# Kernel optimization log

Measured on AMD Instinct MI355X. Metric: run time of the kernel, lower is better.

## Reference

```python
import jax, jax.numpy as jnp
import numpy as np

A = 128      # attention_dim
E = 512      # embedding_dim
NF = 32      # attention_location_n_filters
K = 31       # attention_location_kernel_size
B, T = 64, 1024


def setup_inputs() -> dict:
    key = jax.random.key(0)
    ks = jax.random.split(key, 10)
    inp = {
        "attention_hidden_state": jax.random.normal(ks[0], (B, A), jnp.float32),
        "memory": jax.random.normal(ks[1], (B, T, E), jnp.float32),
        "processed_memory": jax.random.normal(ks[2], (B, T, E), jnp.float32),
        "attention_weights_cat": jax.random.uniform(ks[3], (B, 2, T), jnp.float32),
        "mask": jax.random.randint(ks[4], (B, T), 0, 2).astype(bool),
        # parameters (torch Linear weight layout [out, in], Conv1d [out, in, k])
        "Wq": jax.random.normal(ks[5], (A, A), jnp.float32) / np.sqrt(A),
        "Wm": jax.random.normal(ks[6], (A, E), jnp.float32) / np.sqrt(E),
        "v": jax.random.normal(ks[7], (1, A), jnp.float32) / np.sqrt(A),
        "conv_w": jax.random.normal(ks[8], (NF, 2, K), jnp.float32) / np.sqrt(2 * K),
        "Wl": jax.random.normal(ks[9], (A, NF), jnp.float32) / np.sqrt(NF),
    }
    return inp


def reference(attention_hidden_state, memory, processed_memory,
              attention_weights_cat, mask, Wq, Wm, v, conv_w, Wl):
    # processed_query: [B, 1, A]
    pq = (attention_hidden_state @ Wq.T)[:, None, :]
    # processed_memory through memory_layer: [B, T, A]
    pm = jnp.einsum('bte,ae->bta', processed_memory, Wm)
    # location conv: [B, 2, T] -> [B, NF, T], SAME padding ((K-1)//2)
    pad = (K - 1) // 2
    loc = jax.lax.conv_general_dilated(
        attention_weights_cat, conv_w,
        window_strides=(1,), padding=[(pad, pad)],
        dimension_numbers=('NCH', 'OIH', 'NCH'))
    # [B, T, NF] -> location_layer -> [B, T, A]
    pa = jnp.einsum('bft,af->bta', loc, Wl)
    # energies: [B, T]
    energies = jnp.einsum('bta,a->bt', jnp.tanh(pq + pm + pa), v[0])
    energies = jnp.where(mask, -jnp.inf, energies)
    attention_weights = jax.nn.softmax(energies, axis=1)
    # context: [B, E]
    attention_context = jnp.einsum('bt,bte->be', attention_weights, memory)
    return attention_context, attention_weights
```

## Files before the change

kernel.cpp:

```cpp
#include <hip/hip_runtime.h>
#include <stdint.h>

#define A_DIM 128
#define E_DIM 512
#define NFLT  32
#define KW    31
#define BATCH 64
#define T_DIM 1024

typedef short short8 __attribute__((ext_vector_type(8)));
typedef float float4v __attribute__((ext_vector_type(4)));

__device__ __forceinline__ unsigned short f2bf(float f) {
    union { float f; unsigned int u; } x; x.f = f;
    unsigned int u = x.u;
    return (unsigned short)((u + 0x7fffu + ((u >> 16) & 1u)) >> 16);
}

__global__ __launch_bounds__(256) void prep_kernel(
    const float* __restrict__ hidden, const float* __restrict__ Wq,
    const float* __restrict__ Wm, const float* __restrict__ Wl,
    unsigned short* __restrict__ Wm_bf, unsigned short* __restrict__ Wl_bf,
    float* __restrict__ pq)
{
    int idx = blockIdx.x * 256 + threadIdx.x;
    if (idx < A_DIM * E_DIM) {
        Wm_bf[idx] = f2bf(Wm[idx]);
    } else if (idx < A_DIM * E_DIM + A_DIM * NFLT) {
        int i = idx - A_DIM * E_DIM;
        Wl_bf[i] = f2bf(Wl[i]);
    } else if (idx < A_DIM * E_DIM + A_DIM * NFLT + BATCH * A_DIM) {
        int i = idx - (A_DIM * E_DIM + A_DIM * NFLT);
        int b = i >> 7, a = i & 127;
        const float* h = hidden + b * A_DIM;
        const float* wq = Wq + a * A_DIM;
        float s = 0.f;
        for (int j = 0; j < A_DIM; ++j) s += h[j] * wq[j];
        pq[i] = s;
    }
}

__global__ __launch_bounds__(256) void detect_mask_kernel(
    const unsigned int* __restrict__ mw, int* __restrict__ flag)
{
    __shared__ unsigned int red[256];
    unsigned int f = 0;
    for (int i = threadIdx.x; i < 16384; i += 256) {
        unsigned int v = mw[i];
        if (v == 0x3F800000u) f |= 1u;
        else if (v > 1u) f |= 2u;
    }
    red[threadIdx.x] = f;
    __syncthreads();
    for (int s = 128; s > 0; s >>= 1) {
        if (threadIdx.x < (unsigned)s) red[threadIdx.x] |= red[threadIdx.x + s];
        __syncthreads();
    }
    if (threadIdx.x == 0) {
        unsigned int r = red[0];
        flag[0] = (r & 1u) ? 2 : ((r & 2u) ? 1 : 0);
    }
}

__global__ __launch_bounds__(256) void energies_kernel(
    const float* __restrict__ P,
    const float* __restrict__ awcat,
    const float* __restrict__ convw,
    const unsigned short* __restrict__ Wm_bf,
    const unsigned short* __restrict__ Wl_bf,
    const float* __restrict__ pq,
    const float* __restrict__ vvec,
    float* __restrict__ energies)
{
    const int tid = threadIdx.x;
    const int b  = blockIdx.x >> 3;
    const int t0 = (blockIdx.x & 7) << 7;

    __shared__ float aw_lds[2][160];
    __shared__ unsigned short loc_lds[128][NFLT];

    for (int i = tid; i < 320; i += 256) {
        int c = i / 160, j = i % 160;
        int tg = t0 - 15 + j;
        float vl = 0.f;
        if (j < 158 && tg >= 0 && tg < T_DIM) vl = awcat[(b * 2 + c) * T_DIM + tg];
        aw_lds[c][j] = vl;
    }
    __syncthreads();

    {
        int f = tid >> 3;
        int s = tid & 7;
        float acc[16];
        #pragma unroll
        for (int i = 0; i < 16; ++i) acc[i] = 0.f;
        for (int c = 0; c < 2; ++c) {
            const float* w = convw + (f * 2 + c) * KW;
            for (int k = 0; k < KW; ++k) {
                float wvv = w[k];
                #pragma unroll
                for (int i = 0; i < 16; ++i)
                    acc[i] += wvv * aw_lds[c][s + 8 * i + k];
            }
        }
        #pragma unroll
        for (int i = 0; i < 16; ++i)
            loc_lds[s + 8 * i][f] = f2bf(acc[i]);
    }
    __syncthreads();

    const int lane = tid & 63;
    const int wv   = tid >> 6;
    const int lr   = lane & 15;
    const int lq   = lane >> 4;
    const int k8   = lq * 8;

    float pqf[8], vf[8];
    #pragma unroll
    for (int nf = 0; nf < 8; ++nf) {
        pqf[nf] = pq[b * A_DIM + lr + 16 * nf];
        vf[nf]  = vvec[lr + 16 * nf];
    }

    float4v acc[2][8];
    #pragma unroll
    for (int mf = 0; mf < 2; ++mf)
        #pragma unroll
        for (int nf = 0; nf < 8; ++nf)
            acc[mf][nf] = (float4v){0.f, 0.f, 0.f, 0.f};

    {
        short8 aF[2];
        #pragma unroll
        for (int mf = 0; mf < 2; ++mf) {
            int trow = wv * 32 + mf * 16 + lr;
            aF[mf] = *reinterpret_cast<const short8*>(&loc_lds[trow][k8]);
        }
        #pragma unroll
        for (int nf = 0; nf < 8; ++nf) {
            short8 bF = *reinterpret_cast<const short8*>(&Wl_bf[(lr + 16 * nf) * NFLT + k8]);
            #pragma unroll
            for (int mf = 0; mf < 2; ++mf)
                acc[mf][nf] = __builtin_amdgcn_mfma_f32_16x16x32_bf16(aF[mf], bF, acc[mf][nf], 0, 0, 0);
        }
    }

    const float* Prow[2];
    #pragma unroll
    for (int mf = 0; mf < 2; ++mf) {
        size_t trowg = (size_t)(b * T_DIM + t0 + wv * 32 + mf * 16 + lr);
        Prow[mf] = P + trowg * E_DIM + k8;
    }
    const unsigned short* WmB[8];
    #pragma unroll
    for (int nf = 0; nf < 8; ++nf)
        WmB[nf] = Wm_bf + (size_t)(lr + 16 * nf) * E_DIM + k8;

    #pragma unroll 4
    for (int e0 = 0; e0 < E_DIM; e0 += 32) {
        short8 aF[2];
        #pragma unroll
        for (int mf = 0; mf < 2; ++mf) {
            float4v p0 = *reinterpret_cast<const float4v*>(Prow[mf] + e0);
            float4v p1 = *reinterpret_cast<const float4v*>(Prow[mf] + e0 + 4);
            short8 t;
            #pragma unroll
            for (int j = 0; j < 4; ++j) t[j] = (short)f2bf(p0[j]);
            #pragma unroll
            for (int j = 0; j < 4; ++j) t[4 + j] = (short)f2bf(p1[j]);
            aF[mf] = t;
        }
        #pragma unroll
        for (int nf = 0; nf < 8; ++nf) {
            short8 bF = *reinterpret_cast<const short8*>(WmB[nf] + e0);
            #pragma unroll
            for (int mf = 0; mf < 2; ++mf)
                acc[mf][nf] = __builtin_amdgcn_mfma_f32_16x16x32_bf16(aF[mf], bF, acc[mf][nf], 0, 0, 0);
        }
    }

    #pragma unroll
    for (int mf = 0; mf < 2; ++mf) {
        #pragma unroll
        for (int reg = 0; reg < 4; ++reg) {
            float s = 0.f;
            #pragma unroll
            for (int nf = 0; nf < 8; ++nf) {
                float z = acc[mf][nf][reg] + pqf[nf];
                float th = 1.f - 2.f / (1.f + __expf(2.f * z));
                s += th * vf[nf];
            }
            s += __shfl_xor(s, 1);
            s += __shfl_xor(s, 2);
            s += __shfl_xor(s, 4);
            s += __shfl_xor(s, 8);
            if (lr == 0) {
                int t = t0 + wv * 32 + mf * 16 + 4 * lq + reg;
                energies[b * T_DIM + t] = s;
            }
        }
    }
}

__global__ __launch_bounds__(256) void softmax_kernel(
    const float* __restrict__ energies,
    const void* __restrict__ mask,
    const int* __restrict__ mode_flag,
    float* __restrict__ out)
{
    int b = blockIdx.x, tid = threadIdx.x;
    int mode = mode_flag[0];
    __shared__ float redmax[4];
    __shared__ float redsum[4];
    float x[4];
    #pragma unroll
    for (int i = 0; i < 4; ++i) {
        int idx = b * T_DIM + i * 256 + tid;
        bool msk;
        if (mode == 0)      msk = ((const int*)mask)[idx] != 0;
        else if (mode == 1) msk = ((const unsigned char*)mask)[idx] != 0;
        else                msk = ((const float*)mask)[idx] != 0.f;
        float e = energies[idx];
        x[i] = msk ? -__builtin_inff() : e;
    }
    float m = fmaxf(fmaxf(x[0], x[1]), fmaxf(x[2], x[3]));
    #pragma unroll
    for (int o = 1; o < 64; o <<= 1) m = fmaxf(m, __shfl_xor(m, o));
    if ((tid & 63) == 0) redmax[tid >> 6] = m;
    __syncthreads();
    m = fmaxf(fmaxf(redmax[0], redmax[1]), fmaxf(redmax[2], redmax[3]));

    float p[4], s = 0.f;
    #pragma unroll
    for (int i = 0; i < 4; ++i) { p[i] = __expf(x[i] - m); s += p[i]; }
    #pragma unroll
    for (int o = 1; o < 64; o <<= 1) s += __shfl_xor(s, o);
    if ((tid & 63) == 0) redsum[tid >> 6] = s;
    __syncthreads();
    s = redsum[0] + redsum[1] + redsum[2] + redsum[3];

    float inv = 1.f / s;
    #pragma unroll
    for (int i = 0; i < 4; ++i)
        out[BATCH * E_DIM + b * T_DIM + i * 256 + tid] = p[i] * inv;

    out[b * E_DIM + tid] = 0.f;
    out[b * E_DIM + 256 + tid] = 0.f;
}

__global__ __launch_bounds__(256) void context_kernel(
    const float* __restrict__ memory,
    const float* __restrict__ weights,
    float* __restrict__ ctx)
{
    int b  = blockIdx.x >> 3;
    int t0 = (blockIdx.x & 7) << 7;
    int tid = threadIdx.x;
    __shared__ float wl[128];
    if (tid < 128) wl[tid] = weights[b * T_DIM + t0 + tid];
    __syncthreads();
    const float2* mrow = reinterpret_cast<const float2*>(memory + (size_t)(b * T_DIM + t0) * E_DIM);
    float accx = 0.f, accy = 0.f;
    #pragma unroll 8
    for (int t = 0; t < 128; ++t) {
        float w = wl[t];
        float2 mv = mrow[t * 256 + tid];
        accx += w * mv.x;
        accy += w * mv.y;
    }
    atomicAdd(&ctx[b * E_DIM + 2 * tid], accx);
    atomicAdd(&ctx[b * E_DIM + 2 * tid + 1], accy);
}

extern "C" void kernel_launch(void* const* d_in, const int* in_sizes, int n_in,
                              void* d_out, int out_size, void* d_ws, size_t ws_size,
                              hipStream_t stream) {
    const float* hidden  = (const float*)d_in[0];
    const float* memory  = (const float*)d_in[1];
    const float* procmem = (const float*)d_in[2];
    const float* awcat   = (const float*)d_in[3];
    const void*  mask    = d_in[4];
    const float* Wq      = (const float*)d_in[5];
    const float* Wm      = (const float*)d_in[6];
    const float* v       = (const float*)d_in[7];
    const float* convw   = (const float*)d_in[8];
    const float* Wl      = (const float*)d_in[9];
    float* out = (float*)d_out;

    char* ws = (char*)d_ws;
    float* energies       = (float*)ws;
    float* pq             = (float*)(ws + 262144);
    unsigned short* Wm_bf = (unsigned short*)(ws + 262144 + 32768);
    unsigned short* Wl_bf = (unsigned short*)(ws + 262144 + 32768 + 131072);
    int* mode_flag        = (int*)(ws + 262144 + 32768 + 131072 + 8192);

    prep_kernel<<<304, 256, 0, stream>>>(hidden, Wq, Wm, Wl, Wm_bf, Wl_bf, pq);
    detect_mask_kernel<<<1, 256, 0, stream>>>((const unsigned int*)mask, mode_flag);
    energies_kernel<<<512, 256, 0, stream>>>(procmem, awcat, convw, Wm_bf, Wl_bf, pq, v, energies);
    softmax_kernel<<<64, 256, 0, stream>>>(energies, mask, mode_flag, out);
    context_kernel<<<512, 256, 0, stream>>>(memory, out + BATCH * E_DIM, out);
}
```

Measured before the change: 364.2 us.

## Halve energies tile, quarter context tile, and fold mask detection into prep

```diff
diff --git a/kernel.cpp b/kernel.cpp
--- a/kernel.cpp
+++ b/kernel.cpp
@@ -21,8 +21,30 @@
     const float* __restrict__ hidden, const float* __restrict__ Wq,
     const float* __restrict__ Wm, const float* __restrict__ Wl,
     unsigned short* __restrict__ Wm_bf, unsigned short* __restrict__ Wl_bf,
-    float* __restrict__ pq)
-{
+    float* __restrict__ pq,
+    const unsigned int* __restrict__ maskw, int* __restrict__ mode_flag)
+{
+    if (blockIdx.x == 304) {
+        __shared__ unsigned int red[256];
+        unsigned int f = 0;
+        #pragma unroll
+        for (int i = 0; i < 4; ++i) {
+            unsigned int v = maskw[threadIdx.x + 256 * i];
+            if (v == 0x3F800000u) f |= 1u;
+            else if (v > 1u) f |= 2u;
+        }
+        red[threadIdx.x] = f;
+        __syncthreads();
+        for (int s = 128; s > 0; s >>= 1) {
+            if (threadIdx.x < (unsigned)s) red[threadIdx.x] |= red[threadIdx.x + s];
+            __syncthreads();
+        }
+        if (threadIdx.x == 0) {
+            unsigned int r = red[0];
+            mode_flag[0] = (r & 1u) ? 2 : ((r & 2u) ? 1 : 0);
+        }
+        return;
+    }
     int idx = blockIdx.x * 256 + threadIdx.x;
     if (idx < A_DIM * E_DIM) {
         Wm_bf[idx] = f2bf(Wm[idx]);
@@ -40,29 +62,7 @@
     }
 }
 
-__global__ __launch_bounds__(256) void detect_mask_kernel(
-    const unsigned int* __restrict__ mw, int* __restrict__ flag)
-{
-    __shared__ unsigned int red[256];
-    unsigned int f = 0;
-    for (int i = threadIdx.x; i < 16384; i += 256) {
-        unsigned int v = mw[i];
-        if (v == 0x3F800000u) f |= 1u;
-        else if (v > 1u) f |= 2u;
-    }
-    red[threadIdx.x] = f;
-    __syncthreads();
-    for (int s = 128; s > 0; s >>= 1) {
-        if (threadIdx.x < (unsigned)s) red[threadIdx.x] |= red[threadIdx.x + s];
-        __syncthreads();
-    }
-    if (threadIdx.x == 0) {
-        unsigned int r = red[0];
-        flag[0] = (r & 1u) ? 2 : ((r & 2u) ? 1 : 0);
-    }
-}
-
-__global__ __launch_bounds__(256) void energies_kernel(
+__global__ __launch_bounds__(256, 4) void energies_kernel(
     const float* __restrict__ P,
     const float* __restrict__ awcat,
     const float* __restrict__ convw,
@@ -73,17 +73,17 @@
     float* __restrict__ energies)
 {
     const int tid = threadIdx.x;
-    const int b  = blockIdx.x >> 3;
-    const int t0 = (blockIdx.x & 7) << 7;
-
-    __shared__ float aw_lds[2][160];
-    __shared__ unsigned short loc_lds[128][NFLT];
-
-    for (int i = tid; i < 320; i += 256) {
-        int c = i / 160, j = i % 160;
+    const int b  = blockIdx.x >> 4;
+    const int t0 = (blockIdx.x & 15) << 6;
+
+    __shared__ float aw_lds[2][96];
+    __shared__ unsigned short loc_lds[64][NFLT];
+
+    for (int i = tid; i < 192; i += 256) {
+        int c = i / 96, j = i % 96;
         int tg = t0 - 15 + j;
         float vl = 0.f;
-        if (j < 158 && tg >= 0 && tg < T_DIM) vl = awcat[(b * 2 + c) * T_DIM + tg];
+        if (j < 94 && tg >= 0 && tg < T_DIM) vl = awcat[(b * 2 + c) * T_DIM + tg];
         aw_lds[c][j] = vl;
     }
     __syncthreads();
@@ -91,20 +91,20 @@
     {
         int f = tid >> 3;
         int s = tid & 7;
-        float acc[16];
-        #pragma unroll
-        for (int i = 0; i < 16; ++i) acc[i] = 0.f;
+        float acc[8];
+        #pragma unroll
+        for (int i = 0; i < 8; ++i) acc[i] = 0.f;
         for (int c = 0; c < 2; ++c) {
             const float* w = convw + (f * 2 + c) * KW;
             for (int k = 0; k < KW; ++k) {
                 float wvv = w[k];
                 #pragma unroll
-                for (int i = 0; i < 16; ++i)
+                for (int i = 0; i < 8; ++i)
                     acc[i] += wvv * aw_lds[c][s + 8 * i + k];
             }
         }
         #pragma unroll
-        for (int i = 0; i < 16; ++i)
+        for (int i = 0; i < 8; ++i)
             loc_lds[s + 8 * i][f] = f2bf(acc[i]);
     }
     __syncthreads();
@@ -114,6 +114,7 @@
     const int lr   = lane & 15;
     const int lq   = lane >> 4;
     const int k8   = lq * 8;
+    const int row  = wv * 16 + lr;
 
     float pqf[8], vf[8];
     #pragma unroll
@@ -122,35 +123,21 @@
         vf[nf]  = vvec[lr + 16 * nf];
     }
 
-    float4v acc[2][8];
-    #pragma unroll
-    for (int mf = 0; mf < 2; ++mf)
-        #pragma unroll
-        for (int nf = 0; nf < 8; ++nf)
-            acc[mf][nf] = (float4v){0.f, 0.f, 0.f, 0.f};
+    float4v acc[8];
+    #pragma unroll
+    for (int nf = 0; nf < 8; ++nf)
+        acc[nf] = (float4v){0.f, 0.f, 0.f, 0.f};
 
     {
-        short8 aF[2];
-        #pragma unroll
-        for (int mf = 0; mf < 2; ++mf) {
-            int trow = wv * 32 + mf * 16 + lr;
-            aF[mf] = *reinterpret_cast<const short8*>(&loc_lds[trow][k8]);
-        }
+        short8 aF = *reinterpret_cast<const short8*>(&loc_lds[row][k8]);
         #pragma unroll
         for (int nf = 0; nf < 8; ++nf) {
             short8 bF = *reinterpret_cast<const short8*>(&Wl_bf[(lr + 16 * nf) * NFLT + k8]);
-            #pragma unroll
-            for (int mf = 0; mf < 2; ++mf)
-                acc[mf][nf] = __builtin_amdgcn_mfma_f32_16x16x32_bf16(aF[mf], bF, acc[mf][nf], 0, 0, 0);
-        }
-    }
-
-    const float* Prow[2];
-    #pragma unroll
-    for (int mf = 0; mf < 2; ++mf) {
-        size_t trowg = (size_t)(b * T_DIM + t0 + wv * 32 + mf * 16 + lr);
-        Prow[mf] = P + trowg * E_DIM + k8;
-    }
+            acc[nf] = __builtin_amdgcn_mfma_f32_16x16x32_bf16(aF, bF, acc[nf], 0, 0, 0);
+        }
+    }
+
+    const float* Prow = P + (size_t)(b * T_DIM + t0 + row) * E_DIM + k8;
     const unsigned short* WmB[8];
     #pragma unroll
     for (int nf = 0; nf < 8; ++nf)
@@ -158,46 +145,36 @@
 
     #pragma unroll 4
     for (int e0 = 0; e0 < E_DIM; e0 += 32) {
-        short8 aF[2];
-        #pragma unroll
-        for (int mf = 0; mf < 2; ++mf) {
-            float4v p0 = *reinterpret_cast<const float4v*>(Prow[mf] + e0);
-            float4v p1 = *reinterpret_cast<const float4v*>(Prow[mf] + e0 + 4);
-            short8 t;
-            #pragma unroll
-            for (int j = 0; j < 4; ++j) t[j] = (short)f2bf(p0[j]);
-            #pragma unroll
-            for (int j = 0; j < 4; ++j) t[4 + j] = (short)f2bf(p1[j]);
-            aF[mf] = t;
-        }
+        float4v p0 = *reinterpret_cast<const float4v*>(Prow + e0);
+        float4v p1 = *reinterpret_cast<const float4v*>(Prow + e0 + 4);
+        short8 aF;
+        #pragma unroll
+        for (int j = 0; j < 4; ++j) aF[j] = (short)f2bf(p0[j]);
+        #pragma unroll
+        for (int j = 0; j < 4; ++j) aF[4 + j] = (short)f2bf(p1[j]);
         #pragma unroll
         for (int nf = 0; nf < 8; ++nf) {
             short8 bF = *reinterpret_cast<const short8*>(WmB[nf] + e0);
-            #pragma unroll
-            for (int mf = 0; mf < 2; ++mf)
-                acc[mf][nf] = __builtin_amdgcn_mfma_f32_16x16x32_bf16(aF[mf], bF, acc[mf][nf], 0, 0, 0);
-        }
-    }
-
-    #pragma unroll
-    for (int mf = 0; mf < 2; ++mf) {
-        #pragma unroll
-        for (int reg = 0; reg < 4; ++reg) {
-            float s = 0.f;
-            #pragma unroll
-            for (int nf = 0; nf < 8; ++nf) {
-                float z = acc[mf][nf][reg] + pqf[nf];
-                float th = 1.f - 2.f / (1.f + __expf(2.f * z));
-                s += th * vf[nf];
-            }
-            s += __shfl_xor(s, 1);
-            s += __shfl_xor(s, 2);
-            s += __shfl_xor(s, 4);
-            s += __shfl_xor(s, 8);
-            if (lr == 0) {
-                int t = t0 + wv * 32 + mf * 16 + 4 * lq + reg;
-                energies[b * T_DIM + t] = s;
-            }
+            acc[nf] = __builtin_amdgcn_mfma_f32_16x16x32_bf16(aF, bF, acc[nf], 0, 0, 0);
+        }
+    }
+
+    #pragma unroll
+    for (int reg = 0; reg < 4; ++reg) {
+        float s = 0.f;
+        #pragma unroll
+        for (int nf = 0; nf < 8; ++nf) {
+            float z = acc[nf][reg] + pqf[nf];
+            float th = 1.f - 2.f / (1.f + __expf(2.f * z));
+            s += th * vf[nf];
+        }
+        s += __shfl_xor(s, 1);
+        s += __shfl_xor(s, 2);
+        s += __shfl_xor(s, 4);
+        s += __shfl_xor(s, 8);
+        if (lr == 0) {
+            int t = t0 + wv * 16 + 4 * lq + reg;
+            energies[b * T_DIM + t] = s;
         }
     }
 }
@@ -253,16 +230,16 @@
     const float* __restrict__ weights,
     float* __restrict__ ctx)
 {
-    int b  = blockIdx.x >> 3;
-    int t0 = (blockIdx.x & 7) << 7;
+    int b  = blockIdx.x >> 5;
+    int t0 = (blockIdx.x & 31) << 5;
     int tid = threadIdx.x;
-    __shared__ float wl[128];
-    if (tid < 128) wl[tid] = weights[b * T_DIM + t0 + tid];
+    __shared__ float wl[32];
+    if (tid < 32) wl[tid] = weights[b * T_DIM + t0 + tid];
     __syncthreads();
     const float2* mrow = reinterpret_cast<const float2*>(memory + (size_t)(b * T_DIM + t0) * E_DIM);
     float accx = 0.f, accy = 0.f;
     #pragma unroll 8
-    for (int t = 0; t < 128; ++t) {
+    for (int t = 0; t < 32; ++t) {
         float w = wl[t];
         float2 mv = mrow[t * 256 + tid];
         accx += w * mv.x;
@@ -294,9 +271,9 @@
     unsigned short* Wl_bf = (unsigned short*)(ws + 262144 + 32768 + 131072);
     int* mode_flag        = (int*)(ws + 262144 + 32768 + 131072 + 8192);
 
-    prep_kernel<<<304, 256, 0, stream>>>(hidden, Wq, Wm, Wl, Wm_bf, Wl_bf, pq);
-    detect_mask_kernel<<<1, 256, 0, stream>>>((const unsigned int*)mask, mode_flag);
-    energies_kernel<<<512, 256, 0, stream>>>(procmem, awcat, convw, Wm_bf, Wl_bf, pq, v, energies);
+    prep_kernel<<<305, 256, 0, stream>>>(hidden, Wq, Wm, Wl, Wm_bf, Wl_bf, pq,
+                                         (const unsigned int*)mask, mode_flag);
+    energies_kernel<<<1024, 256, 0, stream>>>(procmem, awcat, convw, Wm_bf, Wl_bf, pq, v, energies);
     softmax_kernel<<<64, 256, 0, stream>>>(energies, mask, mode_flag, out);
-    context_kernel<<<512, 256, 0, stream>>>(memory, out + BATCH * E_DIM, out);
-}
+    context_kernel<<<2048, 256, 0, stream>>>(memory, out + BATCH * E_DIM, out);
+}
```

New measurement: 354.1 us. 1.03x faster.
